# Optimization experiments

Hardware: AMD Instinct MI355X
Metric: run time of the kernel (lower is better)

## Reference

```python
import jax, jax.numpy as jnp
import numpy as np

L_MAX = 3


def setup_inputs() -> dict:
    key = jax.random.key(0)
    k1, k2, k3, k4 = jax.random.split(key, 4)
    B, V, P, Cin, R, Cout = 8, 4096, 32, 64, 2, 128
    N = (L_MAX + 1) ** 2  # 16 spherical-harmonic coeffs
    signal = jax.random.normal(k1, (B, V, Cin), dtype=jnp.float32)
    # gather_nd indices: [..., 0] = batch index, [..., 1] = point index
    bidx = jnp.broadcast_to(jnp.arange(B, dtype=jnp.int32)[:, None, None], (B, V, P))
    pidx = jax.random.randint(k2, (B, V, P), 0, V, dtype=jnp.int32)
    patches_idx = jnp.stack([bidx, pidx], axis=-1)
    conv_kernel = jax.random.normal(k3, (B, V, P, R, N), dtype=jnp.float32)
    kernel_weights = jax.random.normal(k4, (Cout, Cin, R, L_MAX + 1), dtype=jnp.float32)
    biases = jnp.zeros((Cout,), dtype=jnp.float32)
    return {"signal": signal, "patches_idx": patches_idx, "conv_kernel": conv_kernel,
            "kernel_weights": kernel_weights, "biases": biases}


def reference(signal, patches_idx, conv_kernel, kernel_weights, biases):
    l_max = kernel_weights.shape[-1] - 1
    # gather neighbor patches: [B, V, P, Cin]
    patches = signal[patches_idx[..., 0], patches_idx[..., 1]]
    # per-point conv over patch dim: [B, V, Cin, R, N]
    y = jnp.einsum('bvprn,bvpc->bvcrn', conv_kernel, patches)
    y = y * y
    # SH-invariant power per degree l: sum over the 2l+1 orders m
    blocks = []
    p = 0
    for l in range(l_max + 1):
        blocks.append(jnp.sum(y[..., p:p + 2 * l + 1], axis=-1))
        p += 2 * l + 1
    y = jnp.stack(blocks, axis=-1)  # [B, V, Cin, R, l_max+1]
    y = jnp.sqrt(jnp.maximum(y, 1e-4))
    out = jnp.einsum('ijrn,bvjrn->bvi', kernel_weights, y) + biases
    return jax.nn.relu(out)
```

## Files before the change

### kernel.cpp

```cpp
#include <hip/hip_runtime.h>
#include <cstddef>

namespace {

constexpr int kV = 4096;
constexpr int kBlocks = 8 * kV / 16;

typedef float f32x16 __attribute__((ext_vector_type(16)));
typedef float f32x4  __attribute__((ext_vector_type(4)));
typedef short bf16x8 __attribute__((ext_vector_type(8)));

union U8 { unsigned u[4]; uint4 q; bf16x8 v; };

__device__ inline unsigned pk_bf16(float a, float b) {
    unsigned ua = __float_as_uint(a);
    unsigned ub = __float_as_uint(b);
    ua = (ua + 0x7FFFu + ((ua >> 16) & 1u)) >> 16;
    ub = (ub + 0x7FFFu + ((ub >> 16) & 1u)) & 0xFFFF0000u;
    return ua | ub;
}

__global__ void convW(const float* __restrict__ W, unsigned* __restrict__ Wb) {
    const int i = blockIdx.x * 256 + threadIdx.x;
    const float2 w2 = ((const float2*)W)[i];
    Wb[i] = pk_bf16(w2.x, w2.y);
}

__global__ __launch_bounds__(256, 4)
void fused(const float* __restrict__ signal,
           const int* __restrict__ pidx_g,
           const float* __restrict__ ck_g,
           const unsigned short* __restrict__ Wb,
           const float* __restrict__ bias,
           float* __restrict__ out)
{
    __shared__ __align__(16) unsigned short zbf[16][520];
    __shared__ __align__(16) unsigned pS[4][16][64];

    const int t = threadIdx.x;
    const int b = blockIdx.x >> 8;
    const int v_base = (blockIdx.x & 255) * 16;
    const int w    = t >> 6;
    const int lane = t & 63;
    const int n31  = lane & 31;
    const int h    = lane >> 5;
    const int r4   = lane >> 4;
    const int cq   = lane & 15;

    unsigned (*pSw)[64] = pS[w];
    const float* sgb = signal + (size_t)b * kV * 64;

    int vsl[4];
    #pragma unroll
    for (int vg = 0; vg < 4; ++vg)
        vsl[vg] = pidx_g[((((size_t)b * kV + v_base + vg * 4 + w) * 32) + n31) * 2 + 1];

    #pragma unroll
    for (int vg = 0; vg < 4; ++vg) {
        const int g = vg * 4 + w;
        const size_t bv = (size_t)b * kV + (v_base + g);
        const int vsv = vsl[vg];
        const float* ckv = ck_g + bv * 1024;

        float4 S[8];
        #pragma unroll
        for (int k = 0; k < 8; ++k) {
            const int vs = __shfl(vsv, 4 * k + r4);
            S[k] = *(const float4*)(sgb + (size_t)vs * 64 + cq * 4);
        }
        float cA[16];
        #pragma unroll
        for (int j2 = 0; j2 < 4; ++j2) {
            cA[4 * j2 + 0] = ckv[(8 * j2 + h    ) * 32 + n31];
            cA[4 * j2 + 1] = ckv[(8 * j2 + h + 4) * 32 + n31];
            cA[4 * j2 + 2] = ckv[(8 * j2 + h + 2) * 32 + n31];
            cA[4 * j2 + 3] = ckv[(8 * j2 + h + 6) * 32 + n31];
        }

        #pragma unroll
        for (int m = 0; m < 4; ++m) {
            uint4 d;
            d.x = pk_bf16(S[2 * m].x, S[2 * m + 1].x);
            d.y = pk_bf16(S[2 * m].y, S[2 * m + 1].y);
            d.z = pk_bf16(S[2 * m].z, S[2 * m + 1].z);
            d.w = pk_bf16(S[2 * m].w, S[2 * m + 1].w);
            *(uint4*)&pSw[r4 * 4 + m][cq * 4] = d;
        }

        U8 A0, A1;
        #pragma unroll
        for (int j2 = 0; j2 < 4; ++j2) {
            A0.u[j2] = pk_bf16(cA[4 * j2 + 0], cA[4 * j2 + 1]);
            A1.u[j2] = pk_bf16(cA[4 * j2 + 2], cA[4 * j2 + 3]);
        }

        U8 B00, B01, B10, B11;
        #pragma unroll
        for (int j2 = 0; j2 < 4; ++j2) {
            B00.u[j2] = pSw[    4 * h + j2][n31];
            B01.u[j2] = pSw[    4 * h + j2][n31 + 32];
            B10.u[j2] = pSw[8 + 4 * h + j2][n31];
            B11.u[j2] = pSw[8 + 4 * h + j2][n31 + 32];
        }

        f32x16 acc0, acc1;
        #pragma unroll
        for (int j = 0; j < 16; ++j) { acc0[j] = 0.f; acc1[j] = 0.f; }
        acc0 = __builtin_amdgcn_mfma_f32_32x32x16_bf16(A0.v, B00.v, acc0, 0, 0, 0);
        acc1 = __builtin_amdgcn_mfma_f32_32x32x16_bf16(A0.v, B01.v, acc1, 0, 0, 0);
        acc0 = __builtin_amdgcn_mfma_f32_32x32x16_bf16(A1.v, B10.v, acc0, 0, 0, 0);
        acc1 = __builtin_amdgcn_mfma_f32_32x32x16_bf16(A1.v, B11.v, acc1, 0, 0, 0);

        #pragma unroll
        for (int ct = 0; ct < 2; ++ct) {
            const f32x16 a = ct ? acc1 : acc0;
            float s[16];
            #pragma unroll
            for (int j = 0; j < 16; ++j) s[j] = a[j] * a[j];
            const float o00 = s[0], o10 = s[1] + s[2] + s[3];
            const float o20 = s[4], o30 = s[5] + s[6] + s[7];
            const float o01 = s[8], o11 = s[9] + s[10] + s[11];
            const float o21 = s[12], o31 = s[13] + s[14] + s[15];
            const float x0 = s[0] + s[1] + s[2] + s[3];
            const float x1 = s[4] + s[5] + s[6] + s[7];
            const float x2 = s[8] + s[9] + s[10] + s[11];
            const float x3 = s[12] + s[13] + s[14] + s[15];
            const float e0 = __shfl_xor(h ? x0 : o20, 32);
            const float e1 = __shfl_xor(h ? x1 : o30, 32);
            const float e2 = __shfl_xor(h ? x2 : o21, 32);
            const float e3 = __shfl_xor(h ? x3 : o31, 32);
            if (h == 0) {
                const float z00 = sqrtf(fmaxf(o00,      1e-4f));
                const float z10 = sqrtf(fmaxf(o10,      1e-4f));
                const float z20 = sqrtf(fmaxf(o20 + e0, 1e-4f));
                const float z30 = sqrtf(fmaxf(o30 + e1, 1e-4f));
                const float z01 = sqrtf(fmaxf(o01,      1e-4f));
                const float z11 = sqrtf(fmaxf(o11,      1e-4f));
                const float z21 = sqrtf(fmaxf(o21 + e2, 1e-4f));
                const float z31 = sqrtf(fmaxf(o31 + e3, 1e-4f));
                uint4 d;
                d.x = pk_bf16(z00, z10);
                d.y = pk_bf16(z20, z30);
                d.z = pk_bf16(z01, z11);
                d.w = pk_bf16(z21, z31);
                *(uint4*)&zbf[g][(n31 + 32 * ct) * 8] = d;
            }
        }
    }
    __syncthreads();

    const int m15 = lane & 15;
    const int q   = lane >> 4;
    f32x4 pa0, pa1;
    #pragma unroll
    for (int j = 0; j < 4; ++j) { pa0[j] = 0.f; pa1[j] = 0.f; }
    const int i0 = w * 32 + m15;
    const int i1 = w * 32 + 16 + m15;
    #pragma unroll 4
    for (int ks = 0; ks < 16; ++ks) {
        U8 Az, Bw0, Bw1;
        Az.q  = *(const uint4*)&zbf[m15][ks * 32 + q * 8];
        Bw0.q = *(const uint4*)&Wb[(size_t)i0 * 512 + ks * 32 + q * 8];
        Bw1.q = *(const uint4*)&Wb[(size_t)i1 * 512 + ks * 32 + q * 8];
        pa0 = __builtin_amdgcn_mfma_f32_16x16x32_bf16(Az.v, Bw0.v, pa0, 0, 0, 0);
        pa1 = __builtin_amdgcn_mfma_f32_16x16x32_bf16(Az.v, Bw1.v, pa1, 0, 0, 0);
    }
    const float bi0 = bias[i0], bi1 = bias[i1];
    #pragma unroll
    for (int reg = 0; reg < 4; ++reg) {
        const int g = q * 4 + reg;
        const size_t row = ((size_t)b * kV + v_base + g) * 128;
        out[row + i0] = fmaxf(pa0[reg] + bi0, 0.f);
        out[row + i1] = fmaxf(pa1[reg] + bi1, 0.f);
    }
}

}

extern "C" void kernel_launch(void* const* d_in, const int* in_sizes, int n_in,
                              void* d_out, int out_size, void* d_ws, size_t ws_size,
                              hipStream_t stream) {
    const float* signal = (const float*)d_in[0];
    const int*   pidx   = (const int*)d_in[1];
    const float* ck     = (const float*)d_in[2];
    const float* W      = (const float*)d_in[3];
    const float* bias   = (const float*)d_in[4];
    float* out = (float*)d_out;
    unsigned* Wb = (unsigned*)d_ws;

    convW<<<dim3(128), dim3(256), 0, stream>>>(W, Wb);
    fused<<<dim3(kBlocks), dim3(256), 0, stream>>>(
        signal, pidx, ck, (const unsigned short*)Wb, bias, out);
}
```

Baseline: 239.1 us.

## Gather signal rows into LDS via direct global-to-LDS DMA loads

Replaces the per-lane float4 register gathers of neighbor signal rows, and their bf16 packing into LDS, with global_load_lds DMA that writes fp32 rows straight into shared memory. The bf16 conversion now happens when the MFMA B operands are read back from LDS. The conv-kernel coefficient load order is rearranged to match the new k ordering. A block-wide barrier is added inside each of the four per-vertex-group iterations, the fp32 staging buffer doubles the LDS footprint, and the occupancy hint drops from 4 to 3 blocks. The aim is to cut register pressure and VGPR round trips on the gather, at the cost of more barriers and lower occupancy.

```diff
diff --git a/kernel.cpp b/kernel.cpp
--- a/kernel.cpp
+++ b/kernel.cpp
@@ -11,6 +11,13 @@
 typedef short bf16x8 __attribute__((ext_vector_type(8)));
 
 union U8 { unsigned u[4]; uint4 q; bf16x8 v; };
+
+typedef __attribute__((address_space(3))) void lds_void;
+typedef const __attribute__((address_space(1))) void gbl_void;
+
+__device__ inline void dma16(const void* g, void* l) {
+    __builtin_amdgcn_global_load_lds((gbl_void*)g, (lds_void*)l, 16, 0, 0);
+}
 
 __device__ inline unsigned pk_bf16(float a, float b) {
     unsigned ua = __float_as_uint(a);
@@ -26,7 +33,7 @@
     Wb[i] = pk_bf16(w2.x, w2.y);
 }
 
-__global__ __launch_bounds__(256, 4)
+__global__ __launch_bounds__(256, 3)
 void fused(const float* __restrict__ signal,
            const int* __restrict__ pidx_g,
            const float* __restrict__ ck_g,
@@ -34,8 +41,8 @@
            const float* __restrict__ bias,
            float* __restrict__ out)
 {
+    __shared__ __align__(16) float sigS[4][32][64];
     __shared__ __align__(16) unsigned short zbf[16][520];
-    __shared__ __align__(16) unsigned pS[4][16][64];
 
     const int t = threadIdx.x;
     const int b = blockIdx.x >> 8;
@@ -45,9 +52,9 @@
     const int n31  = lane & 31;
     const int h    = lane >> 5;
     const int r4   = lane >> 4;
-    const int cq   = lane & 15;
+    const int c16  = lane & 15;
 
-    unsigned (*pSw)[64] = pS[w];
+    float (*sigSw)[64] = sigS[w];
     const float* sgb = signal + (size_t)b * kV * 64;
 
     int vsl[4];
@@ -62,45 +69,39 @@
         const int vsv = vsl[vg];
         const float* ckv = ck_g + bv * 1024;
 
-        float4 S[8];
         #pragma unroll
-        for (int k = 0; k < 8; ++k) {
-            const int vs = __shfl(vsv, 4 * k + r4);
-            S[k] = *(const float4*)(sgb + (size_t)vs * 64 + cq * 4);
+        for (int i = 0; i < 8; ++i) {
+            const int vs = __shfl(vsv, 4 * i + r4);
+            dma16(sgb + (size_t)vs * 64 + c16 * 4, &sigSw[4 * i][c16 * 4 & 0]);
         }
+
         float cA[16];
         #pragma unroll
-        for (int j2 = 0; j2 < 4; ++j2) {
-            cA[4 * j2 + 0] = ckv[(8 * j2 + h    ) * 32 + n31];
-            cA[4 * j2 + 1] = ckv[(8 * j2 + h + 4) * 32 + n31];
-            cA[4 * j2 + 2] = ckv[(8 * j2 + h + 2) * 32 + n31];
-            cA[4 * j2 + 3] = ckv[(8 * j2 + h + 6) * 32 + n31];
-        }
-
-        #pragma unroll
-        for (int m = 0; m < 4; ++m) {
-            uint4 d;
-            d.x = pk_bf16(S[2 * m].x, S[2 * m + 1].x);
-            d.y = pk_bf16(S[2 * m].y, S[2 * m + 1].y);
-            d.z = pk_bf16(S[2 * m].z, S[2 * m + 1].z);
-            d.w = pk_bf16(S[2 * m].w, S[2 * m + 1].w);
-            *(uint4*)&pSw[r4 * 4 + m][cq * 4] = d;
-        }
+        for (int ks = 0; ks < 2; ++ks)
+            #pragma unroll
+            for (int j2 = 0; j2 < 4; ++j2) {
+                const int p0 = 16 * ks + 8 * h + 2 * j2;
+                cA[ks * 8 + 2 * j2    ] = ckv[(p0    ) * 32 + n31];
+                cA[ks * 8 + 2 * j2 + 1] = ckv[(p0 + 1) * 32 + n31];
+            }
 
         U8 A0, A1;
         #pragma unroll
         for (int j2 = 0; j2 < 4; ++j2) {
-            A0.u[j2] = pk_bf16(cA[4 * j2 + 0], cA[4 * j2 + 1]);
-            A1.u[j2] = pk_bf16(cA[4 * j2 + 2], cA[4 * j2 + 3]);
+            A0.u[j2] = pk_bf16(cA[2 * j2    ], cA[2 * j2 + 1]);
+            A1.u[j2] = pk_bf16(cA[8 + 2 * j2], cA[8 + 2 * j2 + 1]);
         }
+
+        __syncthreads();
 
         U8 B00, B01, B10, B11;
         #pragma unroll
         for (int j2 = 0; j2 < 4; ++j2) {
-            B00.u[j2] = pSw[    4 * h + j2][n31];
-            B01.u[j2] = pSw[    4 * h + j2][n31 + 32];
-            B10.u[j2] = pSw[8 + 4 * h + j2][n31];
-            B11.u[j2] = pSw[8 + 4 * h + j2][n31 + 32];
+            const int p0 = 8 * h + 2 * j2;
+            B00.u[j2] = pk_bf16(sigSw[p0     ][n31     ], sigSw[p0 +  1][n31     ]);
+            B01.u[j2] = pk_bf16(sigSw[p0     ][n31 + 32], sigSw[p0 +  1][n31 + 32]);
+            B10.u[j2] = pk_bf16(sigSw[p0 + 16][n31     ], sigSw[p0 + 17][n31     ]);
+            B11.u[j2] = pk_bf16(sigSw[p0 + 16][n31 + 32], sigSw[p0 + 17][n31 + 32]);
         }
 
         f32x16 acc0, acc1;
```

After: 241.5 us. About the same (+1.0%).
